# Kernel tuning notes

Measured on AMD Instinct MI355X. Metric: run time of the kernel, lower is better.

## Reference

```python
import jax, jax.numpy as jnp
import numpy as np


def conv2d_same(x, w, b):
    # x: (B,C,H,W), w: (O,I,3,3) -> 3x3 'same' conv, stride 1
    y = jax.lax.conv_general_dilated(
        x, w, window_strides=(1, 1), padding=((1, 1), (1, 1)),
        dimension_numbers=("NCHW", "OIHW", "NCHW"))
    return y + b[None, :, None, None]


def setup_inputs() -> dict:
    key = jax.random.key(0)
    ks = jax.random.split(key, 7)
    B, F, E, H, W = 16, 64, 16, 64, 64
    fan2d = F * 9
    state = jax.random.normal(ks[0], (B, F, H, W), dtype=jnp.float32)
    pre_w = jax.random.normal(ks[1], (F, F, 3, 3), dtype=jnp.float32) / np.sqrt(fan2d)
    pre_b = jax.random.normal(ks[2], (F,), dtype=jnp.float32) * 0.01
    attn_w = jax.random.normal(ks[3], (E, F, 3, 3), dtype=jnp.float32) / np.sqrt(fan2d)
    attn_b = jax.random.normal(ks[4], (E,), dtype=jnp.float32) * 0.01
    c3_w = jax.random.normal(ks[5], (F, F), dtype=jnp.float32) / np.sqrt(F)
    c3_b = jax.random.normal(ks[6], (F,), dtype=jnp.float32) * 0.01
    return {"state": state, "pre_w": pre_w, "pre_b": pre_b,
            "attn_w": attn_w, "attn_b": attn_b, "c3_w": c3_w, "c3_b": c3_b}


def reference(state, pre_w, pre_b, attn_w, attn_b, c3_w, c3_b):
    # pre_conv + relu
    x = jax.nn.relu(conv2d_same(state, pre_w, pre_b))
    # visattn_conv + sigmoid -> (B,E,H,W)
    attn = jax.nn.sigmoid(conv2d_same(x, attn_w, attn_b))
    # einsum 'bfyx,beyx->bfeyx'
    x5 = state[:, :, None, :, :] * attn[:, None, :, :, :]  # (B,F,E,H,W)
    # Conv3d kernel (1,1,1) with padding (0,1,1): zero-pad H,W by 1,
    # then pointwise linear over F. Output spatial dims become (E, H+2, W+2).
    x5 = jnp.pad(x5, ((0, 0), (0, 0), (0, 0), (1, 1), (1, 1)))
    y = jnp.einsum("of,bfeyx->boeyx", c3_w, x5) + c3_b[None, :, None, None, None]
    y = jax.nn.relu(y)
    # permute (0,2,1,3,4) then mean over last two dims -> (B,E,F)
    out = jnp.mean(y, axis=(-1, -2)).transpose(0, 2, 1)
    return out, attn
```

## Files before the change

kernel.cpp:

```cpp
#include <hip/hip_runtime.h>
#include <math.h>

constexpr int B = 16, F = 64, E = 16, H = 64, W = 64;
constexpr int XP = 66;
constexpr int CP = 72;
constexpr int YSTRIDE = XP * F;

typedef __bf16 bf16x8 __attribute__((ext_vector_type(8)));
typedef __bf16 bf16x4 __attribute__((ext_vector_type(4)));
typedef float f32x16 __attribute__((ext_vector_type(16)));
typedef float f32x4 __attribute__((ext_vector_type(4)));

__global__ __launch_bounds__(256) void prep_kernel(
    const float* __restrict__ state, const float* __restrict__ pre_w,
    const float* __restrict__ attn_w, const float* __restrict__ c3_w,
    __bf16* __restrict__ xTs, __bf16* __restrict__ wA1,
    __bf16* __restrict__ wA2, __bf16* __restrict__ wT3b,
    float* __restrict__ out0)
{
    __shared__ float s_t[64][68];
    const int blk = blockIdx.x;
    const int tid = threadIdx.x;

    if (blk < 1024) {
        const int b = blk >> 6, y = blk & 63;
        {
            int c = tid >> 2, x0 = (tid & 3) * 16;
            const float* src = state + ((size_t)(b * F + c) * H + y) * W + x0;
            #pragma unroll
            for (int q = 0; q < 4; ++q)
                *(float4*)&s_t[c][x0 + 4 * q] = *(const float4*)(src + 4 * q);
        }
        __syncthreads();
        __bf16* dst = xTs + (size_t)(b * H + y) * YSTRIDE;
        #pragma unroll
        for (int i = 0; i < 2; ++i) {
            int t = tid + i * 256;
            int x = t >> 3, cg = t & 7;
            bf16x8 v;
            #pragma unroll
            for (int j = 0; j < 8; ++j) v[j] = (__bf16)s_t[cg * 8 + j][x];
            *(bf16x8*)(dst + (x + 1) * F + cg * 8) = v;
        }
        if (tid < 16) {
            int bd = tid >> 3, cg = tid & 7;
            bf16x8 z = {};
            *(bf16x8*)(dst + (bd ? 65 : 0) * F + cg * 8) = z;
        }
    } else if (blk < 1168) {
        int idx = (blk - 1024) * 256 + tid;
        if (idx < 64 * 576) {
            int o = idx / 576, rem = idx - o * 576, t = rem >> 6, c = rem & 63;
            wA1[idx] = (__bf16)pre_w[(o * 64 + c) * 9 + t];
        }
        if (idx < 16 * 576) {
            int e = idx / 576, rem = idx - e * 576, t = rem >> 6, c = rem & 63;
            wA2[idx] = (__bf16)attn_w[(e * 64 + c) * 9 + t];
        }
        if (idx < 64 * 64) {
            wT3b[idx] = (__bf16)c3_w[idx];
        }
    } else {
        int idx = (blk - 1168) * 256 + tid;
        float4 z = {0.f, 0.f, 0.f, 0.f};
        *(float4*)(out0 + idx * 4) = z;
    }
}

__global__ __launch_bounds__(256) void mega_kernel(
    const __bf16* __restrict__ xTs, const __bf16* __restrict__ wA1,
    const __bf16* __restrict__ wA2, const __bf16* __restrict__ wT3b,
    const float* __restrict__ pre_b, const float* __restrict__ attn_b,
    const float* __restrict__ c3_b,
    float* __restrict__ attn_out, float* __restrict__ out)
{
    __shared__ __align__(16) char smem[4 * XP * CP * 2];
    const int b = blockIdx.y, yp = blockIdx.x;
    const int tid = threadIdx.x;
    const int wave = tid >> 6, lane = tid & 63;
    const int y0 = yp * 2;

    __bf16* sxo = (__bf16*)smem;
    float (*s_attn)[64][16] = (float(*)[64][16])smem;
    float (*s_sp)[68] = (float(*)[68])(smem + 8192);

    {
        const int n = lane & 31, kh = lane >> 5;
        const int yr = y0 - 1 + wave;
        f32x16 acc[4] = {};
        if (yr >= 0 && yr < H) {
            #pragma unroll
            for (int dy = 0; dy < 3; ++dy) {
                const int row = yr - 1 + dy;
                if (row >= 0 && row < H) {
                    const __bf16* rbase = xTs + (size_t)(b * H + row) * YSTRIDE;
                    #pragma unroll
                    for (int dx = 0; dx < 3; ++dx) {
                        const int t9 = dy * 3 + dx;
                        #pragma unroll
                        for (int cq = 0; cq < 4; ++cq) {
                            const int ko = cq * 16 + kh * 8;
                            bf16x8 a0 = *(const bf16x8*)(wA1 + n * 576 + t9 * 64 + ko);
                            bf16x8 a1 = *(const bf16x8*)(wA1 + (32 + n) * 576 + t9 * 64 + ko);
                            bf16x8 b0 = *(const bf16x8*)(rbase + (n + dx) * F + ko);
                            bf16x8 b1 = *(const bf16x8*)(rbase + (n + dx + 32) * F + ko);
                            acc[0] = __builtin_amdgcn_mfma_f32_32x32x16_bf16(a0, b0, acc[0], 0, 0, 0);
                            acc[1] = __builtin_amdgcn_mfma_f32_32x32x16_bf16(a0, b1, acc[1], 0, 0, 0);
                            acc[2] = __builtin_amdgcn_mfma_f32_32x32x16_bf16(a1, b0, acc[2], 0, 0, 0);
                            acc[3] = __builtin_amdgcn_mfma_f32_32x32x16_bf16(a1, b1, acc[3], 0, 0, 0);
                        }
                    }
                }
            }
            __bf16* orow = sxo + wave * XP * CP;
            #pragma unroll
            for (int mt = 0; mt < 2; ++mt)
                #pragma unroll
                for (int g = 0; g < 4; ++g) {
                    int o0 = mt * 32 + kh * 4 + g * 8;
                    f32x4 b4 = *(const f32x4*)(pre_b + o0);
                    bf16x4 v0, v1;
                    #pragma unroll
                    for (int r = 0; r < 4; ++r) {
                        v0[r] = (__bf16)fmaxf(acc[mt * 2 + 0][g * 4 + r] + b4[r], 0.f);
                        v1[r] = (__bf16)fmaxf(acc[mt * 2 + 1][g * 4 + r] + b4[r], 0.f);
                    }
                    *(bf16x4*)(orow + (n + 1) * CP + o0) = v0;
                    *(bf16x4*)(orow + (n + 33) * CP + o0) = v1;
                }
        } else {
            __bf16* orow = sxo + wave * XP * CP;
            bf16x4 z = {};
            #pragma unroll
            for (int mt = 0; mt < 2; ++mt)
                #pragma unroll
                for (int g = 0; g < 4; ++g) {
                    int o0 = mt * 32 + kh * 4 + g * 8;
                    *(bf16x4*)(orow + (n + 1) * CP + o0) = z;
                    *(bf16x4*)(orow + (n + 33) * CP + o0) = z;
                }
        }
        if (tid < 64) {
            int r = tid >> 4, bd = (tid >> 3) & 1, cg = tid & 7;
            bf16x8 z = {};
            *(bf16x8*)(sxo + (r * XP + (bd ? 65 : 0)) * CP + cg * 8) = z;
        }
    }
    __syncthreads();

    const int rw = wave >> 1, nt2 = wave & 1;
    const int n16 = lane & 15, quad = lane >> 4;
    f32x4 acc2[2] = {};
    {
        const __bf16* aB = wA2 + n16 * 576 + quad * 8;
        #pragma unroll
        for (int dy = 0; dy < 3; ++dy)
            #pragma unroll
            for (int dx = 0; dx < 3; ++dx) {
                const int t9 = dy * 3 + dx;
                #pragma unroll
                for (int cq = 0; cq < 2; ++cq) {
                    bf16x8 a = *(const bf16x8*)(aB + t9 * 64 + cq * 32);
                    #pragma unroll
                    for (int i = 0; i < 2; ++i) {
                        const __bf16* bp = sxo +
                            ((rw + dy) * XP + (nt2 * 32 + i * 16 + n16 + dx)) * CP
                            + quad * 8 + cq * 32;
                        acc2[i] = __builtin_amdgcn_mfma_f32_16x16x32_bf16(
                            a, *(const bf16x8*)bp, acc2[i], 0, 0, 0);
                    }
                }
            }
    }
    __syncthreads();

    #pragma unroll
    for (int i = 0; i < 2; ++i) {
        int x = nt2 * 32 + i * 16 + n16;
        #pragma unroll
        for (int r = 0; r < 4; ++r) {
            int e = quad * 4 + r;
            float val = acc2[i][r] + attn_b[e];
            float sg = 1.f / (1.f + __expf(-val));
            attn_out[((size_t)(b * E + e) * H + (y0 + rw)) * W + x] = sg;
            s_attn[rw][x][e] = sg;
        }
    }
    __syncthreads();

    const int combo = tid & 63;
    const int eg = combo >> 4, og = combo & 15, psub = tid >> 6;
    f32x4 cb4 = ((const f32x4*)c3_b)[og];
    float vsum[4] = {0.f, 0.f, 0.f, 0.f};

    for (int rr = 0; rr < 2; ++rr) {
        {
            const int mt = wave & 1, nt = wave >> 1;
            const int n = lane & 31, kh = lane >> 5;
            const __bf16* bBase = xTs + (size_t)(b * H + y0 + rr) * YSTRIDE
                                  + (nt * 32 + n + 1) * F + kh * 8;
            const __bf16* aBase = wT3b + (mt * 32 + n) * 64 + kh * 8;
            f32x16 acc = {};
            #pragma unroll
            for (int cq = 0; cq < 4; ++cq) {
                bf16x8 a  = *(const bf16x8*)(aBase + cq * 16);
                bf16x8 bb = *(const bf16x8*)(bBase + cq * 16);
                acc = __builtin_amdgcn_mfma_f32_32x32x16_bf16(a, bb, acc, 0, 0, 0);
            }
            #pragma unroll
            for (int g = 0; g < 4; ++g)
                #pragma unroll
                for (int r = 0; r < 4; ++r)
                    s_sp[nt * 32 + n][mt * 32 + kh * 4 + g * 8 + r] = acc[g * 4 + r];
        }
        __syncthreads();

        float accl[4][4] = {};
        #pragma unroll 2
        for (int pp = 0; pp < 16; ++pp) {
            int p = psub * 16 + pp;
            f32x4 a4 = *(const f32x4*)&s_attn[rr][p][eg * 4];
            f32x4 s4 = *(const f32x4*)&s_sp[p][og * 4];
            #pragma unroll
            for (int i = 0; i < 4; ++i)
                #pragma unroll
                for (int j = 0; j < 4; ++j)
                    accl[i][j] += fmaxf(fmaf(a4[i], s4[j], cb4[j]), 0.f);
        }
        __syncthreads();
        float* s_part = &s_sp[0][0];
        #pragma unroll
        for (int i = 0; i < 4; ++i)
            #pragma unroll
            for (int j = 0; j < 4; ++j)
                s_part[(psub * 64 + combo) * 16 + i * 4 + j] = accl[i][j];
        __syncthreads();
        {
            int cmb = tid >> 2, ii = tid & 3;
            #pragma unroll
            for (int j = 0; j < 4; ++j) {
                float v = 0.f;
                #pragma unroll
                for (int ps = 0; ps < 4; ++ps)
                    v += s_part[(ps * 64 + cmb) * 16 + ii * 4 + j];
                vsum[j] += v;
            }
        }
        __syncthreads();
    }
    {
        int cmb = tid >> 2, ii = tid & 3;
        int e = (cmb >> 4) * 4 + ii;
        #pragma unroll
        for (int j = 0; j < 4; ++j) {
            int o = (cmb & 15) * 4 + j;
            float add = vsum[j] * (1.f / 4356.f);
            if (yp == 0) add += 260.f * fmaxf(c3_b[o], 0.f) * (1.f / 4356.f);
            atomicAdd(&out[(b * E + e) * F + o], add);
        }
    }
}

extern "C" void kernel_launch(void* const* d_in, const int* in_sizes, int n_in,
                              void* d_out, int out_size, void* d_ws, size_t ws_size,
                              hipStream_t stream) {
    (void)in_sizes; (void)n_in; (void)out_size; (void)ws_size;
    const float* state  = (const float*)d_in[0];
    const float* pre_w  = (const float*)d_in[1];
    const float* pre_b  = (const float*)d_in[2];
    const float* attn_w = (const float*)d_in[3];
    const float* attn_b = (const float*)d_in[4];
    const float* c3_w   = (const float*)d_in[5];
    const float* c3_b   = (const float*)d_in[6];

    float* out      = (float*)d_out;
    float* attn_out = out + B * E * F;

    char* ws = (char*)d_ws;
    constexpr size_t XT_BYTES = (size_t)B * H * YSTRIDE * 2;
    __bf16* xTs  = (__bf16*)ws;
    __bf16* wA1  = (__bf16*)(ws + XT_BYTES);
    __bf16* wA2  = (__bf16*)(ws + XT_BYTES + 73728);
    __bf16* wT3b = (__bf16*)(ws + XT_BYTES + 73728 + 18432);

    prep_kernel<<<1184, 256, 0, stream>>>(state, pre_w, attn_w, c3_w,
                                          xTs, wA1, wA2, wT3b, out);
    mega_kernel<<<dim3(H / 2, B), 256, 0, stream>>>(xTs, wA1, wA2, wT3b,
                                                    pre_b, attn_b, c3_b,
                                                    attn_out, out);
}
```

Before: 130.1 us.

## Stage pre-conv input rows in LDS instead of reading global per tap

The six input rows needed for the 3x3 pre-conv are first copied into shared memory, zero-padded at the image edges, and the MFMA loop then reads its B operands from LDS instead of global memory for every tap. This removes repeated global loads of overlapping rows across dy/dx taps and the per-row bounds branch. To fit, the shared buffer grows to about 62KB and s_attn/s_sp move to separate offsets, which lowers the number of blocks that can share a CU. A barrier is added before the relu output overwrites the input buffer, and the barrier after conv2 is dropped because s_attn no longer aliases sxo.

```diff
diff --git a/kernel.cpp b/kernel.cpp
--- a/kernel.cpp
+++ b/kernel.cpp
@@ -74,72 +74,75 @@
     const float* __restrict__ c3_b,
     float* __restrict__ attn_out, float* __restrict__ out)
 {
-    __shared__ __align__(16) char smem[4 * XP * CP * 2];
+    __shared__ __align__(16) char smem[63616];
     const int b = blockIdx.y, yp = blockIdx.x;
     const int tid = threadIdx.x;
     const int wave = tid >> 6, lane = tid & 63;
     const int y0 = yp * 2;
 
-    __bf16* sxo = (__bf16*)smem;
-    float (*s_attn)[64][16] = (float(*)[64][16])smem;
-    float (*s_sp)[68] = (float(*)[68])(smem + 8192);
+    __bf16* s_in = (__bf16*)smem;
+    __bf16* sxo  = (__bf16*)smem;
+    float (*s_attn)[64][16] = (float(*)[64][16])(smem + 38016);
+    float (*s_sp)[68] = (float(*)[68])(smem + 46208);
+
+    for (int t = tid; t < 6 * XP * 8; t += 256) {
+        int r = t / (XP * 8), rem = t - r * (XP * 8);
+        int x = rem >> 3, cg = rem & 7;
+        int yy = y0 - 2 + r;
+        bf16x8 v = {};
+        if (yy >= 0 && yy < H)
+            v = *(const bf16x8*)(xTs + (size_t)(b * H + yy) * YSTRIDE + x * F + cg * 8);
+        *(bf16x8*)(s_in + (r * XP + x) * CP + cg * 8) = v;
+    }
+    __syncthreads();
 
     {
         const int n = lane & 31, kh = lane >> 5;
         const int yr = y0 - 1 + wave;
         f32x16 acc[4] = {};
-        if (yr >= 0 && yr < H) {
+        const bool valid = (yr >= 0 && yr < H);
+        if (valid) {
             #pragma unroll
             for (int dy = 0; dy < 3; ++dy) {
-                const int row = yr - 1 + dy;
-                if (row >= 0 && row < H) {
-                    const __bf16* rbase = xTs + (size_t)(b * H + row) * YSTRIDE;
+                #pragma unroll
+                for (int dx = 0; dx < 3; ++dx) {
+                    const int t9 = dy * 3 + dx;
+                    const __bf16* bB = s_in + ((wave + dy) * XP + (n + dx)) * CP + kh * 8;
                     #pragma unroll
-                    for (int dx = 0; dx < 3; ++dx) {
-                        const int t9 = dy * 3 + dx;
-                        #pragma unroll
-                        for (int cq = 0; cq < 4; ++cq) {
-                            const int ko = cq * 16 + kh * 8;
-                            bf16x8 a0 = *(const bf16x8*)(wA1 + n * 576 + t9 * 64 + ko);
-                            bf16x8 a1 = *(const bf16x8*)(wA1 + (32 + n) * 576 + t9 * 64 + ko);
-                            bf16x8 b0 = *(const bf16x8*)(rbase + (n + dx) * F + ko);
-                            bf16x8 b1 = *(const bf16x8*)(rbase + (n + dx + 32) * F + ko);
-                            acc[0] = __builtin_amdgcn_mfma_f32_32x32x16_bf16(a0, b0, acc[0], 0, 0, 0);
-                            acc[1] = __builtin_amdgcn_mfma_f32_32x32x16_bf16(a0, b1, acc[1], 0, 0, 0);
-                            acc[2] = __builtin_amdgcn_mfma_f32_32x32x16_bf16(a1, b0, acc[2], 0, 0, 0);
-                            acc[3] = __builtin_amdgcn_mfma_f32_32x32x16_bf16(a1, b1, acc[3], 0, 0, 0);
-                        }
+                    for (int cq = 0; cq < 4; ++cq) {
+                        const int ko = cq * 16 + kh * 8;
+                        bf16x8 a0 = *(const bf16x8*)(wA1 + n * 576 + t9 * 64 + ko);
+                        bf16x8 a1 = *(const bf16x8*)(wA1 + (32 + n) * 576 + t9 * 64 + ko);
+                        bf16x8 b0 = *(const bf16x8*)(bB + cq * 16);
+                        bf16x8 b1 = *(const bf16x8*)(bB + 32 * CP + cq * 16);
+                        acc[0] = __builtin_amdgcn_mfma_f32_32x32x16_bf16(a0, b0, acc[0], 0, 0, 0);
+                        acc[1] = __builtin_amdgcn_mfma_f32_32x32x16_bf16(a0, b1, acc[1], 0, 0, 0);
+                        acc[2] = __builtin_amdgcn_mfma_f32_32x32x16_bf16(a1, b0, acc[2], 0, 0, 0);
+                        acc[3] = __builtin_amdgcn_mfma_f32_32x32x16_bf16(a1, b1, acc[3], 0, 0, 0);
                     }
                 }
             }
-            __bf16* orow = sxo + wave * XP * CP;
-            #pragma unroll
-            for (int mt = 0; mt < 2; ++mt)
-                #pragma unroll
-                for (int g = 0; g < 4; ++g) {
-                    int o0 = mt * 32 + kh * 4 + g * 8;
-                    f32x4 b4 = *(const f32x4*)(pre_b + o0);
-                    bf16x4 v0, v1;
+        }
+        __syncthreads();
+
+        __bf16* orow = sxo + wave * XP * CP;
+        #pragma unroll
+        for (int mt = 0; mt < 2; ++mt)
+            #pragma unroll
+            for (int g = 0; g < 4; ++g) {
+                int o0 = mt * 32 + kh * 4 + g * 8;
+                f32x4 b4 = *(const f32x4*)(pre_b + o0);
+                bf16x4 v0 = {}, v1 = {};
+                if (valid) {
                     #pragma unroll
                     for (int r = 0; r < 4; ++r) {
                         v0[r] = (__bf16)fmaxf(acc[mt * 2 + 0][g * 4 + r] + b4[r], 0.f);
                         v1[r] = (__bf16)fmaxf(acc[mt * 2 + 1][g * 4 + r] + b4[r], 0.f);
                     }
-                    *(bf16x4*)(orow + (n + 1) * CP + o0) = v0;
-                    *(bf16x4*)(orow + (n + 33) * CP + o0) = v1;
                 }
-        } else {
-            __bf16* orow = sxo + wave * XP * CP;
-            bf16x4 z = {};
-            #pragma unroll
-            for (int mt = 0; mt < 2; ++mt)
-                #pragma unroll
-                for (int g = 0; g < 4; ++g) {
-                    int o0 = mt * 32 + kh * 4 + g * 8;
-                    *(bf16x4*)(orow + (n + 1) * CP + o0) = z;
-                    *(bf16x4*)(orow + (n + 33) * CP + o0) = z;
-                }
-        }
+                *(bf16x4*)(orow + (n + 1) * CP + o0) = v0;
+                *(bf16x4*)(orow + (n + 33) * CP + o0) = v1;
+            }
         if (tid < 64) {
             int r = tid >> 4, bd = (tid >> 3) & 1, cg = tid & 7;
             bf16x8 z = {};
@@ -172,7 +175,6 @@
                 }
             }
     }
-    __syncthreads();
 
     #pragma unroll
     for (int i = 0; i < 2; ++i) {
```

Result: faster. 116.1 us (-10.7%).
